# Kernel optimization log

Hardware: AMD Instinct MI355X
Metric: run time of the kernel (lower is better)

The kernel has to match this reference:

```python
import jax, jax.numpy as jnp
import numpy as np

B, S, E, H = 2, 2048, 1024, 16
D = E // H  # head_dim = 64
SCALE = D ** -0.5


def setup_inputs() -> dict:
    key = jax.random.key(0)
    ks = jax.random.split(key, 5)
    std = E ** -0.5
    return {
        "x": jax.random.normal(ks[0], (B, S, E), dtype=jnp.float32),
        "wq": jax.random.normal(ks[1], (E, E), dtype=jnp.float32) * std,
        "wk": jax.random.normal(ks[2], (E, E), dtype=jnp.float32) * std,
        "wv": jax.random.normal(ks[3], (E, E), dtype=jnp.float32) * std,
        "wo": jax.random.normal(ks[4], (E, E), dtype=jnp.float32) * std,
    }


def reference(x, wq, wk, wv, wo):
    b, s, e = x.shape
    # nn.Linear(bias=False): y = x @ W.T; then split heads -> [B,H,S,D]
    def heads(w):
        return jnp.einsum('bse,fe->bsf', x, w).reshape(b, s, H, D).transpose(0, 2, 1, 3)
    q, k, v = heads(wq), heads(wk), heads(wv)
    attn = jnp.einsum('bhqd,bhkd->bhqk', q, k) * SCALE  # [B,H,S,S]
    attn = jax.nn.softmax(attn, axis=-1)
    out = jnp.einsum('bhqk,bhkd->bhqd', attn, v)        # [B,H,S,D]
    out = out.transpose(0, 2, 1, 3).reshape(b, s, e)
    return jnp.einsum('bse,fe->bsf', out, wo)
```

## Files before the change

### kernel.cpp

```cpp
#include <hip/hip_runtime.h>
#include <stdint.h>

typedef unsigned short ushort_t;
typedef __bf16 bfx8 __attribute__((ext_vector_type(8), may_alias));
typedef __bf16 bfx2 __attribute__((ext_vector_type(2), may_alias));
typedef unsigned short usx8 __attribute__((ext_vector_type(8), may_alias));
typedef unsigned int uix2 __attribute__((ext_vector_type(2), may_alias));
typedef unsigned int uix4 __attribute__((ext_vector_type(4), may_alias));
typedef float f32x2 __attribute__((ext_vector_type(2)));
typedef float f32x4 __attribute__((ext_vector_type(4)));
typedef float f32x4m __attribute__((ext_vector_type(4), may_alias));
typedef float f32x16 __attribute__((ext_vector_type(16)));

#define BB 2
#define SS 2048
#define EE 1024
#define HH 16
#define DD 64
#define MM (BB * SS)
#define XN ((size_t)MM * EE)
#define WN ((size_t)EE * EE)
#define QSCALE 0.18033688011112042f

__device__ __forceinline__ unsigned short f2bf(float f) {
  unsigned int u = __builtin_bit_cast(unsigned int, f);
  u += 0x7fffu + ((u >> 16) & 1u);
  return (unsigned short)(u >> 16);
}

__device__ __forceinline__ usx8 cvt8(const float* p) {
  f32x4m a = *(const f32x4m*)p;
  f32x4m b = *(const f32x4m*)(p + 4);
  usx8 r;
  r[0] = f2bf(a[0]); r[1] = f2bf(a[1]); r[2] = f2bf(a[2]); r[3] = f2bf(a[3]);
  r[4] = f2bf(b[0]); r[5] = f2bf(b[1]); r[6] = f2bf(b[2]); r[7] = f2bf(b[3]);
  return r;
}

__device__ __forceinline__ unsigned int pk2(float lo, float hi) {
  bfx2 t;
  t[0] = (__bf16)lo;
  t[1] = (__bf16)hi;
  return __builtin_bit_cast(unsigned int, t);
}

__device__ __forceinline__ void gl_lds16(const ushort_t* g, ushort_t* l) {
  __builtin_amdgcn_global_load_lds(
      (const __attribute__((address_space(1))) unsigned int*)g,
      (__attribute__((address_space(3))) unsigned int*)l, 16, 0, 0);
}

__global__ __launch_bounds__(256)
void cvt_qkv(const float* __restrict__ x, const float* __restrict__ wq,
             const float* __restrict__ wk, const float* __restrict__ wv,
             ushort_t* __restrict__ dst) {
  size_t i8 = ((size_t)blockIdx.x * 256 + threadIdx.x) * 8;
  const float* s;
  size_t off;
  if (i8 < XN)               { s = x;  off = i8; }
  else if (i8 < XN + WN)     { s = wq; off = i8 - XN; }
  else if (i8 < XN + 2 * WN) { s = wk; off = i8 - XN - WN; }
  else                       { s = wv; off = i8 - XN - 2 * WN; }
  *(usx8*)(dst + i8) = cvt8(s + off);
}

__global__ __launch_bounds__(256)
void cvt_one(const float* __restrict__ s, ushort_t* __restrict__ dst) {
  size_t i8 = ((size_t)blockIdx.x * 256 + threadIdx.x) * 8;
  *(usx8*)(dst + i8) = cvt8(s + i8);
}

__global__ __launch_bounds__(256)
void gemm_qkv(const ushort_t* __restrict__ xb,
              const ushort_t* __restrict__ wqb, const ushort_t* __restrict__ wkb,
              const ushort_t* __restrict__ wvb,
              ushort_t* __restrict__ Qb, ushort_t* __restrict__ Kb,
              ushort_t* __restrict__ Vtb) {
  __shared__ ushort_t As[128 * 32];
  __shared__ ushort_t Bs[128 * 32];

  const int bid = blockIdx.x;
  const ushort_t *A, *W;
  ushort_t* C;
  int bx, by, N;
  float scale = 1.0f;
  if (bid < 512) {
    int t = bid & 255;
    bx = t & 7;  by = t >> 3;
    A = xb;  N = EE;
    if (bid < 256) { W = wqb; C = Qb; scale = QSCALE; }
    else           { W = wkb; C = Kb; }
  } else {
    int t = bid - 512;
    bx = t & 31; by = t >> 5;
    A = wvb; W = xb; C = Vtb; N = MM;
  }
  const int K = EE;

  const int tid = threadIdx.x;
  const int lane = tid & 63;
  const int w = tid >> 6;
  const int l15 = lane & 15, l16 = lane >> 4;
  const int m0 = by * 128;
  const int n0 = bx * 128;
  const int wr = w >> 1, wc = w & 1;

  f32x4 acc[4][4];
#pragma unroll
  for (int i = 0; i < 4; ++i)
#pragma unroll
    for (int j = 0; j < 4; ++j)
#pragma unroll
      for (int r = 0; r < 4; ++r) acc[i][j][r] = 0.0f;

  for (int k0 = 0; k0 < K; k0 += 32) {
#pragma unroll
    for (int q = 0; q < 2; ++q) {
      int c = w * 128 + q * 64 + lane;
      int row = c >> 2, col = c & 3;
      gl_lds16(A + (size_t)(m0 + row) * K + k0 + col * 8,
               As + (size_t)(w * 128 + q * 64) * 8);
      gl_lds16(W + (size_t)(n0 + row) * K + k0 + col * 8,
               Bs + (size_t)(w * 128 + q * 64) * 8);
    }
    __syncthreads();

    bfx8 af[4], bfr[4];
#pragma unroll
    for (int i = 0; i < 4; ++i) {
      int mr = wr * 64 + i * 16 + l15;
      af[i] = *(const bfx8*)(As + mr * 32 + l16 * 8);
      int nr = wc * 64 + i * 16 + l15;
      bfr[i] = *(const bfx8*)(Bs + nr * 32 + l16 * 8);
    }
#pragma unroll
    for (int i = 0; i < 4; ++i)
#pragma unroll
      for (int j = 0; j < 4; ++j)
        acc[i][j] = __builtin_amdgcn_mfma_f32_16x16x32_bf16(af[i], bfr[j],
                                                            acc[i][j], 0, 0, 0);
    __syncthreads();
  }

#pragma unroll
  for (int i = 0; i < 4; ++i) {
    int mr = m0 + wr * 64 + i * 16 + l16 * 4;
#pragma unroll
    for (int j = 0; j < 4; ++j) {
      int nc = n0 + wc * 64 + j * 16 + l15;
#pragma unroll
      for (int r = 0; r < 4; ++r)
        C[(size_t)(mr + r) * N + nc] = f2bf(acc[i][j][r] * scale);
    }
  }
}

__global__ __launch_bounds__(256)
void gemm_o(const ushort_t* __restrict__ A, const ushort_t* __restrict__ W,
            float* __restrict__ C, int M, int N, int K) {
  __shared__ ushort_t As[64 * 32];
  __shared__ ushort_t Bs[128 * 32];

  const int tid = threadIdx.x;
  const int lane = tid & 63;
  const int w = tid >> 6;
  const int l15 = lane & 15, l16 = lane >> 4;
  const int m0 = blockIdx.y * 64;
  const int n0 = blockIdx.x * 128;
  const int wr = w >> 1, wc = w & 1;

  f32x4 acc[2][4];
#pragma unroll
  for (int i = 0; i < 2; ++i)
#pragma unroll
    for (int j = 0; j < 4; ++j)
#pragma unroll
      for (int r = 0; r < 4; ++r) acc[i][j][r] = 0.0f;

  const int ca = w * 64 + lane;
  const int ar = ca >> 2, ac = ca & 3;

  for (int k0 = 0; k0 < K; k0 += 32) {
    gl_lds16(A + (size_t)(m0 + ar) * K + k0 + ac * 8,
             As + (size_t)(w * 64) * 8);
#pragma unroll
    for (int q = 0; q < 2; ++q) {
      int c = w * 128 + q * 64 + lane;
      int row = c >> 2, col = c & 3;
      gl_lds16(W + (size_t)(n0 + row) * K + k0 + col * 8,
               Bs + (size_t)(w * 128 + q * 64) * 8);
    }
    __syncthreads();

    bfx8 af[2], bfr[4];
#pragma unroll
    for (int i = 0; i < 2; ++i) {
      int mr = wr * 32 + i * 16 + l15;
      af[i] = *(const bfx8*)(As + mr * 32 + l16 * 8);
    }
#pragma unroll
    for (int j = 0; j < 4; ++j) {
      int nr = wc * 64 + j * 16 + l15;
      bfr[j] = *(const bfx8*)(Bs + nr * 32 + l16 * 8);
    }
#pragma unroll
    for (int i = 0; i < 2; ++i)
#pragma unroll
      for (int j = 0; j < 4; ++j)
        acc[i][j] = __builtin_amdgcn_mfma_f32_16x16x32_bf16(af[i], bfr[j],
                                                            acc[i][j], 0, 0, 0);
    __syncthreads();
  }

#pragma unroll
  for (int i = 0; i < 2; ++i) {
    int mr = m0 + wr * 32 + i * 16 + l16 * 4;
#pragma unroll
    for (int j = 0; j < 4; ++j) {
      int nc = n0 + wc * 64 + j * 16 + l15;
#pragma unroll
      for (int r = 0; r < 4; ++r)
        C[(size_t)(mr + r) * N + nc] = acc[i][j][r];
    }
  }
}

__global__ __launch_bounds__(64, 2)
void attn_fwd(const ushort_t* Q, const ushort_t* __restrict__ Kg,
              const ushort_t* __restrict__ Vt_g, ushort_t* AO) {
  __shared__ ushort_t Ks[64 * 72];
  __shared__ ushort_t Vs[64 * 72];

  const int lane = threadIdx.x;
  const int l31 = lane & 31, hi = lane >> 5;
  const int n = blockIdx.x;
  const int xcd = n & 7, rr = n >> 3;
  const int g = xcd * 4 + (rr >> 6);
  const int qt = rr & 63;
  const int h = g & 15, b = g >> 4;
  const int q0 = qt * 32;

  const ushort_t* kbase = Kg + (size_t)b * SS * EE + h * DD;
  const ushort_t* vbase = Vt_g + (size_t)h * DD * MM + (size_t)b * SS;

  bfx8 bq[4];
#pragma unroll
  for (int t = 0; t < 4; ++t)
    bq[t] = *(const bfx8*)(Q + (size_t)(b * SS + q0 + l31) * EE + h * DD +
                           t * 16 + hi * 8);

  f32x16 o0, o1;
#pragma unroll
  for (int r = 0; r < 16; ++r) { o0[r] = 0.0f; o1[r] = 0.0f; }
  f32x2 ls2;
  ls2[0] = 0.0f; ls2[1] = 0.0f;

  const int srow = lane >> 3, scol = lane & 7;

  const ushort_t* kp = kbase + (size_t)srow * EE + scol * 8;
  const ushort_t* vp = vbase + (size_t)srow * MM + scol * 8;

  usx8 kreg[8], vreg[8];
#pragma unroll
  for (int i = 0; i < 8; ++i) {
    kreg[i] = *(const usx8*)(kp + (size_t)(8 * i) * EE);
    vreg[i] = *(const usx8*)(vp + (size_t)(8 * i) * MM);
  }

  for (int kt = 0; kt < SS; kt += 64) {
#pragma unroll
    for (int i = 0; i < 8; ++i) {
      *(usx8*)(Ks + (srow + 8 * i) * 72 + scol * 8) = kreg[i];
      *(usx8*)(Vs + (srow + 8 * i) * 72 + scol * 8) = vreg[i];
    }
    if (kt + 64 < SS) {
      kp += (size_t)64 * EE;
      vp += 64;
#pragma unroll
      for (int i = 0; i < 8; ++i) {
        kreg[i] = *(const usx8*)(kp + (size_t)(8 * i) * EE);
        vreg[i] = *(const usx8*)(vp + (size_t)(8 * i) * MM);
      }
    }

    f32x16 pa, pb;
#pragma unroll
    for (int r = 0; r < 16; ++r) { pa[r] = 0.0f; pb[r] = 0.0f; }
    __builtin_amdgcn_s_setprio(1);
#pragma unroll
    for (int t = 0; t < 4; ++t) {
      bfx8 ak0 = *(const bfx8*)(Ks + l31 * 72 + t * 16 + hi * 8);
      bfx8 ak1 = *(const bfx8*)(Ks + (32 + l31) * 72 + t * 16 + hi * 8);
      pa = __builtin_amdgcn_mfma_f32_32x32x16_bf16(ak0, bq[t], pa, 0, 0, 0);
      pb = __builtin_amdgcn_mfma_f32_32x32x16_bf16(ak1, bq[t], pb, 0, 0, 0);
    }
    __builtin_amdgcn_s_setprio(0);

#pragma unroll
    for (int r = 0; r < 16; ++r) {
      pa[r] = __builtin_exp2f(pa[r]);
      pb[r] = __builtin_exp2f(pb[r]);
    }
#pragma unroll
    for (int s = 0; s < 8; ++s) {
      f32x2 ta, tb;
      ta[0] = pa[2 * s]; ta[1] = pa[2 * s + 1];
      tb[0] = pb[2 * s]; tb[1] = pb[2 * s + 1];
      ls2 += ta + tb;
    }

    unsigned int dwA[8], dwB[8];
#pragma unroll
    for (int s = 0; s < 8; ++s) {
      dwA[s] = pk2(pa[2 * s], pa[2 * s + 1]);
      dwB[s] = pk2(pb[2 * s], pb[2 * s + 1]);
    }
    bfx8 fd[4];
#pragma unroll
    for (int g2 = 0; g2 < 2; ++g2) {
      auto sA = __builtin_amdgcn_permlane32_swap(dwA[4 * g2 + 0],
                                                 dwA[4 * g2 + 2], false, false);
      auto sB = __builtin_amdgcn_permlane32_swap(dwA[4 * g2 + 1],
                                                 dwA[4 * g2 + 3], false, false);
      uix4 f;
      f[0] = sA[0]; f[1] = sB[0]; f[2] = sA[1]; f[3] = sB[1];
      fd[g2] = __builtin_bit_cast(bfx8, f);
      auto tA = __builtin_amdgcn_permlane32_swap(dwB[4 * g2 + 0],
                                                 dwB[4 * g2 + 2], false, false);
      auto tB = __builtin_amdgcn_permlane32_swap(dwB[4 * g2 + 1],
                                                 dwB[4 * g2 + 3], false, false);
      uix4 f2;
      f2[0] = tA[0]; f2[1] = tB[0]; f2[2] = tA[1]; f2[3] = tB[1];
      fd[2 + g2] = __builtin_bit_cast(bfx8, f2);
    }

    __builtin_amdgcn_s_setprio(1);
#pragma unroll
    for (int kk = 0; kk < 4; ++kk) {
      bfx8 av0 = *(const bfx8*)(Vs + l31 * 72 + kk * 16 + hi * 8);
      bfx8 av1 = *(const bfx8*)(Vs + (32 + l31) * 72 + kk * 16 + hi * 8);
      o0 = __builtin_amdgcn_mfma_f32_32x32x16_bf16(av0, fd[kk], o0, 0, 0, 0);
      o1 = __builtin_amdgcn_mfma_f32_32x32x16_bf16(av1, fd[kk], o1, 0, 0, 0);
    }
    __builtin_amdgcn_s_setprio(0);
  }

  float lsum = ls2[0] + ls2[1];
  lsum += __shfl_xor(lsum, 32);
  float inv = 1.0f / lsum;

  ushort_t* orow = AO + (size_t)(b * SS + q0 + l31) * EE + h * DD;
#pragma unroll
  for (int g2 = 0; g2 < 4; ++g2) {
    uix2 s0, s1;
    s0[0] = pk2(o0[4 * g2 + 0] * inv, o0[4 * g2 + 1] * inv);
    s0[1] = pk2(o0[4 * g2 + 2] * inv, o0[4 * g2 + 3] * inv);
    *(uix2*)(orow + 8 * g2 + 4 * hi) = s0;
    s1[0] = pk2(o1[4 * g2 + 0] * inv, o1[4 * g2 + 1] * inv);
    s1[1] = pk2(o1[4 * g2 + 2] * inv, o1[4 * g2 + 3] * inv);
    *(uix2*)(orow + 32 + 8 * g2 + 4 * hi) = s1;
  }
}

extern "C" void kernel_launch(void* const* d_in, const int* in_sizes, int n_in,
                              void* d_out, int out_size, void* d_ws, size_t ws_size,
                              hipStream_t stream) {
  const float* x  = (const float*)d_in[0];
  const float* wq = (const float*)d_in[1];
  const float* wk = (const float*)d_in[2];
  const float* wv = (const float*)d_in[3];
  const float* wo = (const float*)d_in[4];
  float* out = (float*)d_out;

  ushort_t* Qb  = (ushort_t*)d_ws;
  ushort_t* Kb  = Qb + XN;
  ushort_t* Vtb = Kb + XN;
  ushort_t* Ab  = Qb;
  ushort_t* S    = (ushort_t*)d_out;
  ushort_t* xb   = S;
  ushort_t* wqb  = S + XN;
  ushort_t* wkb  = S + XN + WN;
  ushort_t* wvb  = S + XN + 2 * WN;
  ushort_t* wob  = Kb;

  dim3 blk(256);
  cvt_qkv<<<dim3((unsigned)((XN + 3 * WN) / (256 * 8))), blk, 0, stream>>>(
      x, wq, wk, wv, S);
  gemm_qkv<<<dim3(768), blk, 0, stream>>>(xb, wqb, wkb, wvb, Qb, Kb, Vtb);
  attn_fwd<<<dim3(2048), dim3(64), 0, stream>>>(Qb, Kb, Vtb, Ab);
  cvt_one<<<dim3((unsigned)(WN / (256 * 8))), blk, 0, stream>>>(wo, wob);
  gemm_o<<<dim3(EE / 128, MM / 64), blk, 0, stream>>>(
      Ab, wob, out, MM, EE, EE);
}
```

Baseline: 205.5 us.

## Share K/V tiles across four waves per block with double-buffered LDS

The attention kernel now runs four waves per 256-thread block, each handling 32 query rows of a 128-row tile. All four waves share the same K/V tiles in LDS, cutting global K/V traffic per query by a factor of four. The tiles are double-buffered across two LDS buffers, so the next tile's global loads overlap compute. The cost is block-wide __syncthreads barriers per tile and fewer, larger blocks (512 instead of 2048), which may change occupancy and latency hiding.

After: 197.6 us. 3.8% less time.

```diff
diff --git a/kernel.cpp b/kernel.cpp
--- a/kernel.cpp
+++ b/kernel.cpp
@@ -225,20 +225,24 @@
   }
 }
 
-__global__ __launch_bounds__(64, 2)
+__global__ __launch_bounds__(256)
 void attn_fwd(const ushort_t* Q, const ushort_t* __restrict__ Kg,
               const ushort_t* __restrict__ Vt_g, ushort_t* AO) {
-  __shared__ ushort_t Ks[64 * 72];
-  __shared__ ushort_t Vs[64 * 72];
-
-  const int lane = threadIdx.x;
+  __shared__ ushort_t Ks0[64 * 72];
+  __shared__ ushort_t Vs0[64 * 72];
+  __shared__ ushort_t Ks1[64 * 72];
+  __shared__ ushort_t Vs1[64 * 72];
+
+  const int tid = threadIdx.x;
+  const int lane = tid & 63;
+  const int w = tid >> 6;
   const int l31 = lane & 31, hi = lane >> 5;
   const int n = blockIdx.x;
   const int xcd = n & 7, rr = n >> 3;
-  const int g = xcd * 4 + (rr >> 6);
-  const int qt = rr & 63;
+  const int g = xcd * 4 + (rr >> 4);
+  const int qt = rr & 15;
   const int h = g & 15, b = g >> 4;
-  const int q0 = qt * 32;
+  const int q0 = qt * 128 + w * 32;
 
   const ushort_t* kbase = Kg + (size_t)b * SS * EE + h * DD;
   const ushort_t* vbase = Vt_g + (size_t)h * DD * MM + (size_t)b * SS;
@@ -255,42 +259,30 @@
   f32x2 ls2;
   ls2[0] = 0.0f; ls2[1] = 0.0f;
 
-  const int srow = lane >> 3, scol = lane & 7;
-
-  const ushort_t* kp = kbase + (size_t)srow * EE + scol * 8;
-  const ushort_t* vp = vbase + (size_t)srow * MM + scol * 8;
-
-  usx8 kreg[8], vreg[8];
-#pragma unroll
-  for (int i = 0; i < 8; ++i) {
-    kreg[i] = *(const usx8*)(kp + (size_t)(8 * i) * EE);
-    vreg[i] = *(const usx8*)(vp + (size_t)(8 * i) * MM);
-  }
-
-  for (int kt = 0; kt < SS; kt += 64) {
-#pragma unroll
-    for (int i = 0; i < 8; ++i) {
-      *(usx8*)(Ks + (srow + 8 * i) * 72 + scol * 8) = kreg[i];
-      *(usx8*)(Vs + (srow + 8 * i) * 72 + scol * 8) = vreg[i];
-    }
-    if (kt + 64 < SS) {
-      kp += (size_t)64 * EE;
-      vp += 64;
-#pragma unroll
-      for (int i = 0; i < 8; ++i) {
-        kreg[i] = *(const usx8*)(kp + (size_t)(8 * i) * EE);
-        vreg[i] = *(const usx8*)(vp + (size_t)(8 * i) * MM);
-      }
-    }
-
+  const int r0 = tid >> 3, c0 = tid & 7;
+
+  usx8 k0r, k1r, v0r, v1r;
+  auto load_t = [&](int key0) {
+    k0r = *(const usx8*)(kbase + (size_t)(key0 + r0) * EE + c0 * 8);
+    k1r = *(const usx8*)(kbase + (size_t)(key0 + r0 + 32) * EE + c0 * 8);
+    v0r = *(const usx8*)(vbase + (size_t)r0 * MM + key0 + c0 * 8);
+    v1r = *(const usx8*)(vbase + (size_t)(r0 + 32) * MM + key0 + c0 * 8);
+  };
+  auto write_t = [&](ushort_t* Ksb, ushort_t* Vsb) {
+    *(usx8*)(Ksb + r0 * 72 + c0 * 8) = k0r;
+    *(usx8*)(Ksb + (r0 + 32) * 72 + c0 * 8) = k1r;
+    *(usx8*)(Vsb + r0 * 72 + c0 * 8) = v0r;
+    *(usx8*)(Vsb + (r0 + 32) * 72 + c0 * 8) = v1r;
+  };
+  auto compute_t = [&](const ushort_t* Ksb, const ushort_t* Vsb) {
     f32x16 pa, pb;
 #pragma unroll
     for (int r = 0; r < 16; ++r) { pa[r] = 0.0f; pb[r] = 0.0f; }
     __builtin_amdgcn_s_setprio(1);
 #pragma unroll
     for (int t = 0; t < 4; ++t) {
-      bfx8 ak0 = *(const bfx8*)(Ks + l31 * 72 + t * 16 + hi * 8);
-      bfx8 ak1 = *(const bfx8*)(Ks + (32 + l31) * 72 + t * 16 + hi * 8);
+      bfx8 ak0 = *(const bfx8*)(Ksb + l31 * 72 + t * 16 + hi * 8);
+      bfx8 ak1 = *(const bfx8*)(Ksb + (32 + l31) * 72 + t * 16 + hi * 8);
       pa = __builtin_amdgcn_mfma_f32_32x32x16_bf16(ak0, bq[t], pa, 0, 0, 0);
       pb = __builtin_amdgcn_mfma_f32_32x32x16_bf16(ak1, bq[t], pb, 0, 0, 0);
     }
@@ -337,12 +329,29 @@
     __builtin_amdgcn_s_setprio(1);
 #pragma unroll
     for (int kk = 0; kk < 4; ++kk) {
-      bfx8 av0 = *(const bfx8*)(Vs + l31 * 72 + kk * 16 + hi * 8);
-      bfx8 av1 = *(const bfx8*)(Vs + (32 + l31) * 72 + kk * 16 + hi * 8);
+      bfx8 av0 = *(const bfx8*)(Vsb + l31 * 72 + kk * 16 + hi * 8);
+      bfx8 av1 = *(const bfx8*)(Vsb + (32 + l31) * 72 + kk * 16 + hi * 8);
       o0 = __builtin_amdgcn_mfma_f32_32x32x16_bf16(av0, fd[kk], o0, 0, 0, 0);
       o1 = __builtin_amdgcn_mfma_f32_32x32x16_bf16(av1, fd[kk], o1, 0, 0, 0);
     }
     __builtin_amdgcn_s_setprio(0);
+  };
+
+  load_t(0);
+  write_t(Ks0, Vs0);
+  __syncthreads();
+
+  for (int kt = 0; kt < SS; kt += 128) {
+    load_t(kt + 64);
+    compute_t(Ks0, Vs0);
+    write_t(Ks1, Vs1);
+    __syncthreads();
+    if (kt + 128 < SS) load_t(kt + 128);
+    compute_t(Ks1, Vs1);
+    if (kt + 128 < SS) {
+      write_t(Ks0, Vs0);
+      __syncthreads();
+    }
   }
 
   float lsum = ls2[0] + ls2[1];
@@ -387,7 +396,7 @@
   cvt_qkv<<<dim3((unsigned)((XN + 3 * WN) / (256 * 8))), blk, 0, stream>>>(
       x, wq, wk, wv, S);
   gemm_qkv<<<dim3(768), blk, 0, stream>>>(xb, wqb, wkb, wvb, Qb, Kb, Vtb);
-  attn_fwd<<<dim3(2048), dim3(64), 0, stream>>>(Qb, Kb, Vtb, Ab);
+  attn_fwd<<<dim3(512), blk, 0, stream>>>(Qb, Kb, Vtb, Ab);
   cvt_one<<<dim3((unsigned)(WN / (256 * 8))), blk, 0, stream>>>(wo, wob);
   gemm_o<<<dim3(EE / 128, MM / 64), blk, 0, stream>>>(
       Ab, wob, out, MM, EE, EE);
```
